# Kernel tuning notes

Hardware: AMD Instinct MI355X
Metric: run time of the kernel (lower is better)

## Reference

```python
import jax, jax.numpy as jnp
import numpy as np

NDIR = 5    # directions (hardcoded range(5) in torch forward)
E = 16      # num_experts
W = 3       # local_window (neighbors per expert, includes self)
D = 128     # expert_dim
P = 256     # patches per expert (equal-size partition of num_patches)
B = 4       # batch
DEPTH = 8   # cantor_depth


def _cantor_coord(pos, max_len, depth):
    x = pos / max(1, max_len - 1)
    x = max(1e-06, min(x, 1.0 - 1e-06))
    val, factor = 0.0, 0.5
    for _ in range(depth):
        x *= 3.0
        digit = int(x)
        x -= digit
        if digit == 2:
            val += factor
        factor *= 0.5
    return val

# Static routing table (buffer in the torch module): W nearest experts by
# |cantor coord| distance; neighbor projections are visited in ascending
# expert-id order in the torch loop, hence the sort.
_coords = np.array([_cantor_coord(i, E, DEPTH) for i in range(E)], dtype=np.float32)
_routes = np.zeros((E, W), dtype=np.int32)
for _i in range(E):
    _d = np.abs(_coords - _coords[_i])
    _routes[_i] = np.sort(np.argsort(_d, kind='stable')[:W])
ROUTES = jnp.asarray(_routes)  # [E, W]


def setup_inputs() -> dict:
    key = jax.random.key(0)
    k1, k2, k3, k4 = jax.random.split(key, 4)
    return {
        'Q_aff': jax.random.normal(k1, (NDIR, E, B, P), jnp.float32),
        'K_aff': jax.random.normal(k2, (NDIR, E, B, P), jnp.float32),
        'V': jax.random.normal(k3, (NDIR, E, B, P, D), jnp.float32),
        'betas': jax.random.normal(k4, (E, E), jnp.float32),
        'temperature': jnp.ones((1,), jnp.float32),
        'fusion_weights': jnp.ones((NDIR,), jnp.float32) / NDIR,
    }


def reference(Q_aff, K_aff, V, betas, temperature, fusion_weights):
    routes = ROUTES                                   # [E, W]
    # Gather neighbor K affinities / values per expert (replaces pad/stack loop).
    K_n = K_aff[:, routes]                            # [NDIR, E, W, B, P]
    V_n = V[:, routes]                                # [NDIR, E, W, B, P, D]
    K_nb = jnp.transpose(K_n, (0, 1, 3, 2, 4))        # [NDIR, E, B, W, P]
    temp = jnp.abs(temperature[0]) + 1e-06
    # scores[x,e,b,p,w,q] = Q[x,e,b,p] * K_neighbor[x,e,b,w,q] / temp
    scores = Q_aff[:, :, :, :, None, None] * K_nb[:, :, :, None, :, :] / temp
    # Cross-expert edges are scaled by sigmoid(beta); self edges are not.
    is_self = routes == jnp.arange(E)[:, None]        # [E, W]
    beta_fac = jnp.where(is_self, 1.0,
                         jax.nn.sigmoid(betas[jnp.arange(E)[:, None], routes]))
    scores = scores * beta_fac[None, :, None, None, :, None]
    attn = jax.nn.softmax(scores.reshape(NDIR, E, B, P, W * P), axis=-1)
    V_flat = jnp.transpose(V_n, (0, 1, 3, 2, 4, 5)).reshape(NDIR, E, B, W * P, D)
    attended = jnp.einsum('xebpk,xebkf->xebpf', attn, V_flat)  # [NDIR,E,B,P,D]
    # Expert e owns contiguous patches [e*P, (e+1)*P) -> scatter is a reshape.
    attended = jnp.transpose(attended, (0, 2, 1, 3, 4)).reshape(NDIR, B, E * P, D)
    wts = jax.nn.softmax(fusion_weights)
    return jnp.einsum('x,xbnf->bnf', wts, attended)   # [B, E*P, D]
```

## Files before the change

### kernel.cpp

```cpp
#include <hip/hip_runtime.h>
#include <math.h>

#define NDIR 5
#define E_ 16
#define W_ 3
#define D_ 128
#define P_ 256
#define B_ 4
#define ROWS 64
#define NPQ 4
#define NT 12
#define PARTN (B_ * E_ * NPQ * ROWS * D_)

typedef __attribute__((ext_vector_type(8))) short short8;
typedef __attribute__((ext_vector_type(4))) float f32x4;
typedef __attribute__((ext_vector_type(8))) float f32x8;
typedef __attribute__((ext_vector_type(4))) _Float16 half4;

struct RoutesArg { int r[E_][W_]; };

static RoutesArg make_routes() {
    float coords[E_];
    for (int i = 0; i < E_; ++i) {
        double x = (double)i / (double)(E_ - 1);
        if (x < 1e-6) x = 1e-6;
        if (x > 1.0 - 1e-6) x = 1.0 - 1e-6;
        double val = 0.0, factor = 0.5;
        for (int d = 0; d < 8; ++d) {
            x *= 3.0;
            int digit = (int)x;
            x -= (double)digit;
            if (digit == 2) val += factor;
            factor *= 0.5;
        }
        coords[i] = (float)val;
    }
    RoutesArg R;
    for (int i = 0; i < E_; ++i) {
        float d[E_]; int idx[E_];
        for (int j = 0; j < E_; ++j) { d[j] = fabsf(coords[j] - coords[i]); idx[j] = j; }
        for (int a = 1; a < E_; ++a) {
            int key = idx[a]; float kd = d[key];
            int c = a - 1;
            while (c >= 0 && d[idx[c]] > kd) { idx[c + 1] = idx[c]; --c; }
            idx[c + 1] = key;
        }
        int top[W_] = { idx[0], idx[1], idx[2] };
        if (top[0] > top[1]) { int t = top[0]; top[0] = top[1]; top[1] = t; }
        if (top[1] > top[2]) { int t = top[1]; top[1] = top[2]; top[2] = t; }
        if (top[0] > top[1]) { int t = top[0]; top[0] = top[1]; top[1] = t; }
        for (int w = 0; w < W_; ++w) R.r[i][w] = top[w];
    }
    return R;
}

static __device__ __forceinline__ unsigned short f2bf(float f) {
    union { float f; unsigned int u; } v; v.f = f;
    unsigned int r = (v.u + 0x7FFFu + ((v.u >> 16) & 1u)) >> 16;
    return (unsigned short)r;
}

static __device__ __forceinline__ unsigned int cvt_pk_bf16(float lo, float hi) {
    unsigned int r;
    asm("v_cvt_pk_bf16_f32 %0, %1, %2" : "=v"(r) : "v"(lo), "v"(hi));
    return r;
}

static __device__ __forceinline__ short8 pack8(f32x8 a) {
    union { unsigned int u[4]; short8 s; } cv;
    cv.u[0] = cvt_pk_bf16(a[0], a[1]);
    cv.u[1] = cvt_pk_bf16(a[2], a[3]);
    cv.u[2] = cvt_pk_bf16(a[4], a[5]);
    cv.u[3] = cvt_pk_bf16(a[6], a[7]);
    return cv.s;
}

static __device__ __forceinline__ void gld16(const void* g, void* l) {
    __builtin_amdgcn_global_load_lds(
        (const __attribute__((address_space(1))) unsigned int*)g,
        (__attribute__((address_space(3))) unsigned int*)l,
        16, 0, 0);
}

__global__ __launch_bounds__(256) void vt_prep_kernel(
    const float* __restrict__ V, unsigned short* __restrict__ Vt)
{
    __shared__ unsigned short tl[32][80];

    const int slab = blockIdx.x >> 2;
    const int kq   = blockIdx.x & 3;
    const int tid  = threadIdx.x;

    const float* src = V + (size_t)slab * (P_ * D_) + (size_t)(kq * 64) * D_;
    unsigned short* dst = Vt + (size_t)slab * (P_ * D_) + kq * 64;

    #pragma unroll
    for (int ft = 0; ft < 4; ++ft) {
        const int f0 = ft * 32;
        if (ft) __syncthreads();
        #pragma unroll
        for (int it = 0; it < 2; ++it) {
            const int idx = it * 256 + tid;
            const int kk  = idx >> 3;
            const int fg  = idx & 7;
            const float4 v = *reinterpret_cast<const float4*>(
                src + (size_t)kk * D_ + f0 + fg * 4);
            tl[fg * 4 + 0][kk] = f2bf(v.x);
            tl[fg * 4 + 1][kk] = f2bf(v.y);
            tl[fg * 4 + 2][kk] = f2bf(v.z);
            tl[fg * 4 + 3][kk] = f2bf(v.w);
        }
        __syncthreads();
        {
            const int f  = tid >> 3;
            const int kg = tid & 7;
            const uint4 val = *reinterpret_cast<const uint4*>(&tl[f][kg * 8]);
            *reinterpret_cast<uint4*>(&dst[(size_t)(f0 + f) * P_ + kg * 8]) = val;
        }
    }
}

template <bool ATOMIC>
__global__ __launch_bounds__(256, 4) void cantor_partial3_kernel(
    const float* __restrict__ Q, const float* __restrict__ K,
    const unsigned short* __restrict__ Vt, const float* __restrict__ betas,
    const float* __restrict__ temperature, const float* __restrict__ fusion,
    void* __restrict__ target, RoutesArg routes)
{
    __shared__ float s_lds[W_ * P_];
    __shared__ __align__(16) unsigned char vbuf[16384];

    const int orig = blockIdx.x;
    const int wg   = (orig & 7) * 160 + (orig >> 3);

    const int pq = wg & 3;
    const int b  = (wg >> 2) & 3;
    const int e  = (wg >> 4) & 15;
    const int x  = wg >> 8;

    const int tid  = threadIdx.x;
    const int lane = tid & 63;
    const int wv   = tid >> 6;
    const int l15  = lane & 15;
    const int lg   = lane >> 4;

    const int rowbase = (wv >> 1) * 32;
    const int fhalf   = wv & 1;

    const int phase = orig % NT;

    const float temp = fabsf(temperature[0]) + 1e-6f;

    float fwx;
    {
        float fv[NDIR], fmx = -1e30f, fsum = 0.f;
        #pragma unroll
        for (int i = 0; i < NDIR; ++i) { fv[i] = fusion[i]; fmx = fmaxf(fmx, fv[i]); }
        #pragma unroll
        for (int i = 0; i < NDIR; ++i) { fv[i] = __expf(fv[i] - fmx); fsum += fv[i]; }
        fwx = fv[x] / fsum;
    }

    int rt[W_]; float bf3[W_];
    #pragma unroll
    for (int w = 0; w < W_; ++w) {
        rt[w] = routes.r[e][w];
        float bv_ = betas[e * E_ + rt[w]];
        bf3[w] = (rt[w] == e) ? 1.0f : 1.0f / (1.0f + __expf(-bv_));
    }

    #pragma unroll
    for (int w = 0; w < W_; ++w)
        s_lds[w * P_ + tid] =
            K[(((size_t)(x * E_ + rt[w])) * B_ + b) * P_ + tid] * bf3[w];

    const float* Qb = Q + (((size_t)(x * E_ + e)) * B_ + b) * P_ + pq * ROWS + rowbase;
    float q2[2];
    q2[0] = Qb[l15] / temp;
    q2[1] = Qb[16 + l15] / temp;

    const unsigned short* vs0 = Vt + ((size_t)(x * E_ + rt[0]) * B_ + b) * (P_ * D_);
    const unsigned short* vs1 = Vt + ((size_t)(x * E_ + rt[1]) * B_ + b) * (P_ * D_);
    const unsigned short* vs2 = Vt + ((size_t)(x * E_ + rt[2]) * B_ + b) * (P_ * D_);

    const int src_off = (wv * 8 + (lane >> 3)) * P_ + ((lane & 7) ^ (lane >> 3)) * 8;

    const int rdbase = fhalf * 8192 + l15 * 128 + ((lg ^ (l15 & 7)) * 16);

    #define STAGE(t_) do {                                                       \
        const unsigned short* sl_ = ((t_) >> 2) == 0 ? vs0                       \
                                  : (((t_) >> 2) == 1 ? vs1 : vs2);              \
        const unsigned short* sb_ = sl_ + (((t_) & 3) * 64) + src_off;           \
        char* db_ = (char*)vbuf + wv * 1024;                                     \
        gld16(sb_,          db_);                                                \
        gld16(sb_ +  8192,  db_ + 4096);                                         \
        gld16(sb_ + 16384,  db_ + 8192);                                         \
        gld16(sb_ + 24576,  db_ + 12288);                                        \
    } while (0)

    STAGE(phase);
    __syncthreads();

    f32x4 acc[2][4];
    #pragma unroll
    for (int fr = 0; fr < 2; ++fr)
        #pragma unroll
        for (int c = 0; c < 4; ++c)
            acc[fr][c] = (f32x4){0.f, 0.f, 0.f, 0.f};
    float den[2] = {0.f, 0.f};

    #pragma unroll 1
    for (int tt = 0; tt < NT; ++tt) {
        int t = tt + phase;
        if (t >= NT) t -= NT;

        #pragma unroll
        for (int s = 0; s < 2; ++s) {
            const float* sp = s_lds + (t >> 2) * P_ + (t & 3) * 64 + s * 32 + 8 * lg;
            f32x8 sv;
            {
                const float4 s0_ = *reinterpret_cast<const float4*>(sp);
                const float4 s1_ = *reinterpret_cast<const float4*>(sp + 4);
                sv[0] = s0_.x; sv[1] = s0_.y; sv[2] = s0_.z; sv[3] = s0_.w;
                sv[4] = s1_.x; sv[5] = s1_.y; sv[6] = s1_.z; sv[7] = s1_.w;
            }
            short8 af0, af1;
            {
                f32x8 e0, e1;
                #pragma unroll
                for (int i = 0; i < 8; ++i) e0[i] = __expf(q2[0] * sv[i]);
                #pragma unroll
                for (int i = 0; i < 8; ++i) e1[i] = __expf(q2[1] * sv[i]);
                den[0] += ((e0[0]+e0[1]) + (e0[2]+e0[3])) + ((e0[4]+e0[5]) + (e0[6]+e0[7]));
                den[1] += ((e1[0]+e1[1]) + (e1[2]+e1[3])) + ((e1[4]+e1[5]) + (e1[6]+e1[7]));
                af0 = pack8(e0);
                af1 = pack8(e1);
            }

            #pragma unroll
            for (int c = 0; c < 4; ++c) {
                const short8 bf = *reinterpret_cast<const short8*>(
                    &vbuf[(rdbase ^ (s << 6)) + c * 2048]);
                acc[0][c] = __builtin_amdgcn_mfma_f32_16x16x32_bf16(
                    af0, bf, acc[0][c], 0, 0, 0);
                acc[1][c] = __builtin_amdgcn_mfma_f32_16x16x32_bf16(
                    af1, bf, acc[1][c], 0, 0, 0);
            }
        }
        if (tt < NT - 1) {
            int tn = t + 1;
            if (tn >= NT) tn -= NT;
            __syncthreads();
            STAGE(tn);
            __syncthreads();
        }
    }
    #undef STAGE

    #pragma unroll
    for (int fr = 0; fr < 2; ++fr) {
        den[fr] += __shfl_xor(den[fr], 16);
        den[fr] += __shfl_xor(den[fr], 32);
    }

    const size_t obase = ((((size_t)b * E_ + e) * NPQ) + pq) * (ROWS * D_);

    #pragma unroll
    for (int fr = 0; fr < 2; ++fr) {
        #pragma unroll
        for (int r = 0; r < 4; ++r) {
            const float dr = __shfl(den[fr], 4 * lg + r);
            const float sc = fwx / dr;
            const int row = rowbase + fr * 16 + 4 * lg + r;
            const size_t off = obase + (size_t)row * D_ + fhalf * 64;
            #pragma unroll
            for (int c = 0; c < 4; ++c) {
                const float v = sc * acc[fr][c][r];
                if (ATOMIC) {
                    atomicAdd((float*)target + off + c * 16 + l15, v);
                } else {
                    _Float16* op = (_Float16*)target + (size_t)x * PARTN + off;
                    op[c * 16 + l15] = (_Float16)v;
                }
            }
        }
    }
}

__global__ __launch_bounds__(256) void reduce5h_kernel(
    const _Float16* __restrict__ part, float* __restrict__ out)
{
    const size_t i = (size_t)blockIdx.x * 256 + threadIdx.x;
    float a0 = 0.f, a1 = 0.f, a2 = 0.f, a3 = 0.f;
    #pragma unroll
    for (int x = 0; x < NDIR; ++x) {
        const half4 h = *reinterpret_cast<const half4*>(part + (size_t)x * PARTN + i * 4);
        a0 += (float)h[0]; a1 += (float)h[1]; a2 += (float)h[2]; a3 += (float)h[3];
    }
    reinterpret_cast<float4*>(out)[i] = make_float4(a0, a1, a2, a3);
}

extern "C" void kernel_launch(void* const* d_in, const int* in_sizes, int n_in,
                              void* d_out, int out_size, void* d_ws, size_t ws_size,
                              hipStream_t stream) {
    (void)in_sizes; (void)n_in;
    RoutesArg R = make_routes();
    const float* Q     = (const float*)d_in[0];
    const float* K     = (const float*)d_in[1];
    const float* V     = (const float*)d_in[2];
    const float* betas = (const float*)d_in[3];
    const float* tempr = (const float*)d_in[4];
    const float* fuse  = (const float*)d_in[5];
    float* out = (float*)d_out;

    const size_t vt_bytes   = (size_t)NDIR * E_ * B_ * P_ * D_ * 2;
    const size_t part_bytes = (size_t)NDIR * PARTN * 2;

    dim3 grid(NDIR * E_ * B_ * NPQ);
    dim3 block(256);

    if (ws_size >= vt_bytes + part_bytes) {
        unsigned short* Vt = (unsigned short*)d_ws;
        _Float16* part = (_Float16*)((char*)d_ws + vt_bytes);
        hipLaunchKernelGGL(vt_prep_kernel, dim3(1280), block, 0, stream, V, Vt);
        hipLaunchKernelGGL((cantor_partial3_kernel<false>), grid, block, 0, stream,
                           Q, K, Vt, betas, tempr, fuse, (void*)part, R);
        hipLaunchKernelGGL(reduce5h_kernel, dim3(2048), block, 0, stream,
                           part, out);
    } else {
        unsigned short* Vt = (unsigned short*)d_ws;
        (void)hipMemsetAsync(d_out, 0, (size_t)out_size * 4, stream);
        hipLaunchKernelGGL(vt_prep_kernel, dim3(1280), block, 0, stream, V, Vt);
        hipLaunchKernelGGL((cantor_partial3_kernel<true>), grid, block, 0, stream,
                           Q, K, Vt, betas, tempr, fuse, (void*)out, R);
    }
}
```

Measured before the change: 56.45 us.

## Double-buffer V tiles in LDS with prefetch two steps ahead

Replaces the single 16KB V staging buffer with two buffers, so the tile for step t+2 is loaded asynchronously while step t is computed. Partial vmcnt waits and raw s_barrier replace the two __syncthreads per iteration. The per-block phase rotation of tile order is dropped, so all blocks now walk tiles in the same order. This doubles LDS use, which may reduce occupancy, and it relies on hand-written waitcnt counts being correct.

```diff
diff --git a/kernel.cpp b/kernel.cpp
--- a/kernel.cpp
+++ b/kernel.cpp
@@ -128,7 +128,7 @@
     void* __restrict__ target, RoutesArg routes)
 {
     __shared__ float s_lds[W_ * P_];
-    __shared__ __align__(16) unsigned char vbuf[16384];
+    __shared__ __align__(16) unsigned char vbuf[2][16384];
 
     const int orig = blockIdx.x;
     const int wg   = (orig & 7) * 160 + (orig >> 3);
@@ -147,8 +147,6 @@
     const int rowbase = (wv >> 1) * 32;
     const int fhalf   = wv & 1;
 
-    const int phase = orig % NT;
-
     const float temp = fabsf(temperature[0]) + 1e-6f;
 
     float fwx;
@@ -187,18 +185,19 @@
 
     const int rdbase = fhalf * 8192 + l15 * 128 + ((lg ^ (l15 & 7)) * 16);
 
-    #define STAGE(t_) do {                                                       \
+    #define STAGE(bi, t_) do {                                                   \
         const unsigned short* sl_ = ((t_) >> 2) == 0 ? vs0                       \
                                   : (((t_) >> 2) == 1 ? vs1 : vs2);              \
         const unsigned short* sb_ = sl_ + (((t_) & 3) * 64) + src_off;           \
-        char* db_ = (char*)vbuf + wv * 1024;                                     \
+        char* db_ = (char*)vbuf[bi] + wv * 1024;                                 \
         gld16(sb_,          db_);                                                \
         gld16(sb_ +  8192,  db_ + 4096);                                         \
         gld16(sb_ + 16384,  db_ + 8192);                                         \
         gld16(sb_ + 24576,  db_ + 12288);                                        \
     } while (0)
 
-    STAGE(phase);
+    STAGE(0, 0);
+    STAGE(1, 1);
     __syncthreads();
 
     f32x4 acc[2][4];
@@ -210,9 +209,8 @@
     float den[2] = {0.f, 0.f};
 
     #pragma unroll 1
-    for (int tt = 0; tt < NT; ++tt) {
-        int t = tt + phase;
-        if (t >= NT) t -= NT;
+    for (int t = 0; t < NT; ++t) {
+        const int cur = t & 1;
 
         #pragma unroll
         for (int s = 0; s < 2; ++s) {
@@ -240,19 +238,23 @@
             #pragma unroll
             for (int c = 0; c < 4; ++c) {
                 const short8 bf = *reinterpret_cast<const short8*>(
-                    &vbuf[(rdbase ^ (s << 6)) + c * 2048]);
+                    &vbuf[cur][(rdbase ^ (s << 6)) + c * 2048]);
                 acc[0][c] = __builtin_amdgcn_mfma_f32_16x16x32_bf16(
                     af0, bf, acc[0][c], 0, 0, 0);
                 acc[1][c] = __builtin_amdgcn_mfma_f32_16x16x32_bf16(
                     af1, bf, acc[1][c], 0, 0, 0);
             }
         }
-        if (tt < NT - 1) {
-            int tn = t + 1;
-            if (tn >= NT) tn -= NT;
-            __syncthreads();
-            STAGE(tn);
-            __syncthreads();
+
+        __builtin_amdgcn_s_barrier();
+        if (t + 2 < NT) STAGE(cur, t + 2);
+        if (t + 1 < NT) {
+            if (t + 2 < NT) {
+                asm volatile("s_waitcnt vmcnt(4)" ::: "memory");
+            } else {
+                asm volatile("s_waitcnt vmcnt(0)" ::: "memory");
+            }
+            __builtin_amdgcn_s_barrier();
         }
     }
     #undef STAGE
```

Result: faster. 54.77 us (-3.0%).
